# Performance work log

Hardware: AMD Instinct MI355X
Metric: run time of the kernel (lower is better)

The kernel has to match this reference:

```python
import jax, jax.numpy as jnp
import numpy as np
import math

B, LQ, S, D = 8, 4096, 77, 1024
H, HD = 16, 64
R, ALPHA = 192, 16.0
LORA_SCALE = ALPHA / R
N_SUBJ = 32


def setup_inputs() -> dict:
    key = jax.random.key(0)
    ks = jax.random.split(key, 16)
    w = 0.02
    return {
        "hidden_states": jax.random.normal(ks[0], (B, LQ, D), jnp.float32),
        "encoder_hidden_states": jax.random.normal(ks[1], (B, S, D), jnp.float32),
        "Wq": jax.random.normal(ks[2], (D, D), jnp.float32) * w,
        "Wk": jax.random.normal(ks[3], (D, D), jnp.float32) * w,
        "Wv": jax.random.normal(ks[4], (D, D), jnp.float32) * w,
        "Wo": jax.random.normal(ks[5], (D, D), jnp.float32) * w,
        "bo": jnp.zeros((D,), jnp.float32),
        "Ak": jax.random.normal(ks[6], (R, D), jnp.float32) * w,
        "Bk": jax.random.normal(ks[7], (D, R), jnp.float32) * w,
        "Av": jax.random.normal(ks[8], (R, D), jnp.float32) * w,
        "Bv": jax.random.normal(ks[9], (D, R), jnp.float32) * w,
        "Ao": jax.random.normal(ks[10], (R, D), jnp.float32) * w,
        "Bo": jax.random.normal(ks[11], (D, R), jnp.float32) * w,
        "cross_attn_scale_factor": jnp.ones((), jnp.float32),
        "subj_b": jax.random.randint(ks[12], (N_SUBJ,), 0, B, jnp.int32),
        "subj_n": jax.random.randint(ks[13], (N_SUBJ,), 0, S, jnp.int32),
    }


def _lora(x, A, Bm):
    # peft LoRA delta: scale * (x @ A^T) @ B^T
    return LORA_SCALE * ((x @ A.T) @ Bm.T)


def reference(hidden_states, encoder_hidden_states, Wq, Wk, Wv, Wo, bo,
              Ak, Bk, Av, Bv, Ao, Bo, cross_attn_scale_factor, subj_b, subj_n):
    hs, ehs = hidden_states, encoder_hidden_states
    # q_lora_updates_query=False -> query uses the base projection only
    q = hs @ Wq.T                                  # [B, LQ, D]
    k = ehs @ Wk.T + _lora(ehs, Ak, Bk)            # [B, S, D] (to_k_lora)
    v = ehs @ Wv.T + _lora(ehs, Av, Bv)            # [B, S, D] (to_v_lora)

    q = q.reshape(B, LQ, H, HD).transpose(0, 2, 1, 3)   # [B,H,LQ,HD]
    k = k.reshape(B, S, H, HD).transpose(0, 2, 1, 3)    # [B,H,S,HD]
    v = v.reshape(B, S, H, HD).transpose(0, 2, 1, 3)

    scale = 1.0 / math.sqrt(HD)
    attn_score = jnp.einsum('bhld,bhsd->bhls', q, k) * scale  # [B,H,LQ,S]

    # normalize_cross_attn: zero-center subject-token scores over query dim,
    # then rescale by the learned cross_attn_scale_factor.
    sub = attn_score[subj_b, :, :, subj_n]                    # [K,H,LQ]
    sub = (sub - sub.mean(axis=2, keepdims=True)) * cross_attn_scale_factor
    attn_score = attn_score.at[subj_b, :, :, subj_n].set(sub)

    attn_weight = jax.nn.softmax(attn_score, axis=-1)
    out = jnp.einsum('bhls,bhsd->bhld', attn_weight, v)       # [B,H,LQ,HD]
    out = out.transpose(0, 2, 1, 3).reshape(B, LQ, D)

    # to_out_lora: base out-proj (with bias) + LoRA delta; to_out[1] dropout = id
    out = out @ Wo.T + bo + _lora(out, Ao, Bo)
    return out
```

## Files before the change

### kernel.cpp

```cpp
#include <hip/hip_runtime.h>
#include <stdint.h>

#define B_     8
#define LQ_    4096
#define S_     77
#define SP_    80
#define D_     1024
#define H_     16
#define HD_    64
#define NC_    1280
#define NSUBJ_ 32

typedef __attribute__((ext_vector_type(4))) float  f4;
typedef __attribute__((ext_vector_type(8))) short  short8;
typedef __attribute__((ext_vector_type(8))) unsigned short us8;
typedef __attribute__((ext_vector_type(4))) unsigned short us4;

__device__ __forceinline__ unsigned short f2bf(float f) {
  union { float f; unsigned u; } x; x.f = f;
  unsigned r = x.u + 0x7FFFu + ((x.u >> 16) & 1u);
  return (unsigned short)(r >> 16);
}

__device__ __forceinline__ void gload16(const void* g, void* s) {
  __builtin_amdgcn_global_load_lds((const __attribute__((address_space(1))) void*)g,
                                   (__attribute__((address_space(3))) void*)s, 16, 0, 0);
}

__global__ __launch_bounds__(256) void k_hssum(const float* __restrict__ hs,
                                               float* __restrict__ part,
                                               unsigned short* __restrict__ hsb) {
  int b = blockIdx.y;
  size_t base = ((size_t)b * LQ_ + (size_t)blockIdx.x * 64) * D_ + threadIdx.x * 4;
  f4 acc = {0.f, 0.f, 0.f, 0.f};
  for (int l = 0; l < 64; ++l) {
    f4 v = *(const f4*)(hs + base + (size_t)l * D_);
    acc += v;
    if (hsb) {
      us4 o;
#pragma unroll
      for (int j = 0; j < 4; ++j) o[j] = f2bf(v[j]);
      *(us4*)(hsb + base + (size_t)l * D_) = o;
    }
  }
  *(f4*)(part + (size_t)blockIdx.x * (B_ * D_) + b * D_ + threadIdx.x * 4) = acc;
}

__global__ __launch_bounds__(256) void k_hsred(const float* __restrict__ part,
                                               float* __restrict__ hssum) {
  int i = blockIdx.x * 256 + threadIdx.x;
  float s = 0.f;
  for (int x = 0; x < 64; ++x) s += part[(size_t)x * (B_ * D_) + i];
  hssum[i] = s;
}

__global__ __launch_bounds__(256) void k_tr4(const float* __restrict__ Wq, const float* __restrict__ Ak,
                                             const float* __restrict__ Av, const float* __restrict__ Ao,
                                             float* __restrict__ wqT, float* __restrict__ akT,
                                             float* __restrict__ avT, float* __restrict__ aoT) {
  int z = blockIdx.z;
  const float* in = z == 0 ? Wq : (z == 1 ? Ak : (z == 2 ? Av : Ao));
  float* out = z == 0 ? wqT : (z == 1 ? akT : (z == 2 ? avT : aoT));
  int R = z == 0 ? 1024 : 192;
  const int C = 1024;
  int c0 = blockIdx.x * 32, r0 = blockIdx.y * 32;
  if (r0 >= R) return;
  __shared__ float tile[32][33];
  int tx = threadIdx.x & 31, ty = threadIdx.x >> 5;
#pragma unroll
  for (int k = 0; k < 4; ++k)
    tile[ty + 8 * k][tx] = in[(size_t)(r0 + ty + 8 * k) * C + c0 + tx];
  __syncthreads();
#pragma unroll
  for (int k = 0; k < 4; ++k)
    out[(size_t)(c0 + ty + 8 * k) * R + r0 + tx] = tile[tx][ty + 8 * k];
}

template <bool OBF>
__device__ __forceinline__ void gemm64_body(
    const float* __restrict__ A, int lda, const float* __restrict__ Bt, int ldb,
    void* __restrict__ Cv, int ldc, long cbase, const float* __restrict__ Dm, int ldd,
    int M, int Mv, int N, int K, float alpha, int m0, int n0,
    short* As, short* Bs) {
  int t = threadIdx.x, lane = t & 63, wid = t >> 6;
  int wm = wid >> 1, wn = wid & 1;
  f4 acc[2][2] = {};
  int srow = t >> 2, skc = (t & 3) * 8;
  for (int k0 = 0; k0 < K; k0 += 32) {
    __syncthreads();
    f4 a0 = {0,0,0,0}, a1 = {0,0,0,0}, b0 = {0,0,0,0}, b1 = {0,0,0,0};
    if (m0 + srow < Mv) {
      const float* p = A + (size_t)(m0 + srow) * lda + k0 + skc;
      a0 = *(const f4*)p; a1 = *(const f4*)(p + 4);
    }
    if (n0 + srow < N) {
      const float* p = Bt + (size_t)(n0 + srow) * ldb + k0 + skc;
      b0 = *(const f4*)p; b1 = *(const f4*)(p + 4);
    }
    us8 ua, ub;
#pragma unroll
    for (int j = 0; j < 4; ++j) {
      ua[j] = f2bf(a0[j]); ua[4 + j] = f2bf(a1[j]);
      ub[j] = f2bf(b0[j]); ub[4 + j] = f2bf(b1[j]);
    }
    *(us8*)(As + srow * 40 + skc) = ua;
    *(us8*)(Bs + srow * 40 + skc) = ub;
    __syncthreads();
    short8 fa[2], fb[2];
#pragma unroll
    for (int i = 0; i < 2; ++i) {
      fa[i] = *(const short8*)(As + (wm * 32 + i * 16 + (lane & 15)) * 40 + (lane >> 4) * 8);
      fb[i] = *(const short8*)(Bs + (wn * 32 + i * 16 + (lane & 15)) * 40 + (lane >> 4) * 8);
    }
#pragma unroll
    for (int mi = 0; mi < 2; ++mi)
#pragma unroll
      for (int ni = 0; ni < 2; ++ni)
        acc[mi][ni] = __builtin_amdgcn_mfma_f32_16x16x32_bf16(fa[mi], fb[ni], acc[mi][ni], 0, 0, 0);
  }
#pragma unroll
  for (int mi = 0; mi < 2; ++mi)
#pragma unroll
    for (int ni = 0; ni < 2; ++ni)
#pragma unroll
      for (int j = 0; j < 4; ++j) {
        int row = m0 + wm * 32 + mi * 16 + (lane >> 4) * 4 + j;
        int col = n0 + wn * 32 + ni * 16 + (lane & 15);
        if (row < M && col < N) {
          float val = acc[mi][ni][j] * alpha;
          if (Dm) val += Dm[(size_t)row * ldd + col];
          size_t idx = (size_t)cbase + (size_t)row * ldc + col;
          if (OBF) ((unsigned short*)Cv)[idx] = f2bf(val);
          else     ((float*)Cv)[idx] = val;
        }
      }
}

template <bool OBF>
__global__ __launch_bounds__(256) void k_gemm_small(
    const float* __restrict__ A, int lda, long sA1, long sA2,
    const float* __restrict__ Bt, int ldb, long sB1, long sB2,
    void* __restrict__ Cv, int ldc, long sC1, long sC2,
    const float* __restrict__ Dm, int ldd,
    int M, int Mv, int N, int K, float alpha, int Z2) {
  int z = blockIdx.z, z1 = z / Z2, z2 = z - z1 * Z2;
  __shared__ short As[64 * 40];
  __shared__ short Bs[64 * 40];
  gemm64_body<OBF>(A + z1 * sA1 + z2 * sA2, lda, Bt + z1 * sB1 + z2 * sB2, ldb,
                   Cv, ldc, z1 * sC1 + z2 * sC2, Dm, ldd, M, Mv, N, K, alpha,
                   blockIdx.x * 64, blockIdx.y * 64, As, Bs);
}

__global__ __launch_bounds__(256) void k_weff(
    const float* __restrict__ Bk, const float* __restrict__ Bv, const float* __restrict__ Bo,
    const float* __restrict__ akT, const float* __restrict__ avT, const float* __restrict__ aoT,
    const float* __restrict__ Wk, const float* __restrict__ Wv, const float* __restrict__ Wo,
    float* __restrict__ weff, float alpha) {
  int z = blockIdx.z;
  const float* A  = z == 0 ? Bk : (z == 1 ? Bv : Bo);
  const float* Bt = z == 0 ? akT : (z == 1 ? avT : aoT);
  const float* Dm = z == 0 ? Wk : (z == 1 ? Wv : Wo);
  __shared__ short As[64 * 40];
  __shared__ short Bs[64 * 40];
  gemm64_body<false>(A, 192, Bt, 192, weff + (size_t)z * 1048576, 1024, 0, Dm, 1024,
                     1024, 1024, 1024, 192, alpha, blockIdx.x * 64, blockIdx.y * 64, As, Bs);
}

__global__ void k_mubeta(const float* __restrict__ hssum, const float* __restrict__ Wq,
                         const float* __restrict__ kv,
                         const int* __restrict__ sb, const int* __restrict__ sn,
                         const float* __restrict__ csf_p,
                         float* __restrict__ alphav, float* __restrict__ betav) {
  int h = blockIdx.x, b = blockIdx.y;
  int t = threadIdx.x;
  __shared__ float qp[64];
  {
    int hd = t >> 1, half = t & 1;
    const float* wr = Wq + (size_t)(h * 64 + hd) * D_ + half * 512;
    const float* hp = hssum + b * D_ + half * 512;
    float s = 0.f;
    for (int d = 0; d < 512; d += 4) {
      f4 w = *(const f4*)(wr + d);
      f4 x = *(const f4*)(hp + d);
      s += w[0] * x[0] + w[1] * x[1] + w[2] * x[2] + w[3] * x[3];
    }
    s += __shfl_xor(s, 1, 64);
    if (half == 0) qp[hd] = s * (1.f / 4096.f);
  }
  __syncthreads();
  int s = t;
  if (s >= SP_) return;
  const float* kp = kv + ((size_t)(b * SP_ + s)) * 2048 + h * HD_;
  float mu = 0.f;
#pragma unroll 8
  for (int hd = 0; hd < HD_; ++hd) mu += qp[hd] * kp[hd];
  mu *= 0.125f;
  bool subj = false;
  for (int i = 0; i < NSUBJ_; ++i) subj = subj || (sb[i] == b && sn[i] == s);
  float csf = *csf_p;
  int c = b * NC_ + h * SP_ + s;
  alphav[c] = subj ? csf : 1.f;
  betav[c] = (s >= S_) ? -1e30f : (subj ? -mu * csf : 0.f);
}

__global__ __launch_bounds__(512, 4) void k_score_big(
    const unsigned short* __restrict__ hsb, const unsigned short* __restrict__ Mt,
    const float* __restrict__ alphav, const float* __restrict__ betav,
    unsigned short* __restrict__ P) {
  extern __shared__ short lds[];
  short* A0 = lds;
  short* B0 = lds + 16384;
  int id = blockIdx.x;
  int x = id & 7, idp = id >> 3;
  int nt = idp & 7;
  int pid = (idp >> 3) * 8 + x;
  int b = pid >> 4, mt = pid & 15;
  int m0 = mt * 256, n0 = nt * 160;

  const unsigned short* Ab = hsb + (size_t)b * LQ_ * D_;
  const unsigned short* Bb = Mt + (size_t)b * NC_ * D_;
  const float* alp = alphav + b * NC_;
  const float* bet = betav + b * NC_;
  unsigned short* Pb = P + (size_t)b * LQ_ * NC_;

  int t = threadIdx.x, lane = t & 63, wid = t >> 6;
  int wm = wid >> 1, wn = wid & 1;
  int r = lane & 15, q = lane >> 4;
  f4 acc[4][5] = {};

  auto SA = [&](int bf, int k0, int p) {
    int cb = p * 512 + wid * 64;
    int cc = cb + lane;
    int row = cc >> 2, gc = (cc & 3) ^ ((row >> 1) & 3);
    gload16(Ab + (size_t)(m0 + row) * D_ + k0 + gc * 8, (char*)(A0 + bf * 8192) + cb * 16);
  };
  auto SB = [&](int bf, int k0, int p) {
    int cb = p * 512 + wid * 64;
    int cc = cb + lane;
    int row = cc >> 2, gc = (cc & 3) ^ ((row >> 1) & 3);
    gload16(Bb + (size_t)(n0 + row) * D_ + k0 + gc * 8, (char*)(B0 + bf * 5120) + cb * 16);
  };
  auto STAGE = [&](int bf, int k0) {
    SA(bf, k0, 0); SA(bf, k0, 1);
    SB(bf, k0, 0);
    if (wid < 2) SB(bf, k0, 1);
  };

  STAGE(0, 0);
  int cur = 0;
  for (int kt = 0; kt < 32; ++kt) {
    if (kt < 31) {
      STAGE(cur ^ 1, (kt + 1) * 32);
      if (wid < 2) asm volatile("s_waitcnt vmcnt(4)" ::: "memory");
      else         asm volatile("s_waitcnt vmcnt(3)" ::: "memory");
    } else {
      asm volatile("s_waitcnt vmcnt(0)" ::: "memory");
    }
    __builtin_amdgcn_s_barrier();
    const short* Ar = A0 + cur * 8192;
    const short* Br = B0 + cur * 5120;
    short8 fa[4], fb[5];
#pragma unroll
    for (int ni = 0; ni < 5; ++ni) {
      int row = wn * 80 + ni * 16 + r;
      fb[ni] = *(const short8*)(Br + row * 32 + ((q ^ ((row >> 1) & 3)) * 8));
    }
#pragma unroll
    for (int mi = 0; mi < 4; ++mi) {
      int row = wm * 64 + mi * 16 + r;
      fa[mi] = *(const short8*)(Ar + row * 32 + ((q ^ ((row >> 1) & 3)) * 8));
    }
    __builtin_amdgcn_s_setprio(1);
#pragma unroll
    for (int mi = 0; mi < 4; ++mi)
#pragma unroll
      for (int ni = 0; ni < 5; ++ni)
        acc[mi][ni] = __builtin_amdgcn_mfma_f32_16x16x32_bf16(fa[mi], fb[ni], acc[mi][ni], 0, 0, 0);
    __builtin_amdgcn_s_setprio(0);
    __builtin_amdgcn_s_barrier();
    cur ^= 1;
  }

  float al[5], be[5];
#pragma unroll
  for (int ni = 0; ni < 5; ++ni) {
    int cc = n0 + wn * 80 + ni * 16 + r;
    al[ni] = alp[cc]; be[ni] = bet[cc];
  }
#pragma unroll
  for (int mi = 0; mi < 4; ++mi) {
#pragma unroll
    for (int j = 0; j < 4; ++j) {
      float v[5];
      float m = -3.0e38f;
#pragma unroll
      for (int ni = 0; ni < 5; ++ni) { v[ni] = acc[mi][ni][j] * al[ni] + be[ni]; m = fmaxf(m, v[ni]); }
#pragma unroll
      for (int off = 1; off < 16; off <<= 1) m = fmaxf(m, __shfl_xor(m, off, 64));
      float ssum = 0.f;
#pragma unroll
      for (int ni = 0; ni < 5; ++ni) { v[ni] = __expf(v[ni] - m); ssum += v[ni]; }
#pragma unroll
      for (int off = 1; off < 16; off <<= 1) ssum += __shfl_xor(ssum, off, 64);
      float inv = 1.f / ssum;
      int row = m0 + wm * 64 + mi * 16 + q * 4 + j;
      size_t rb = (size_t)row * NC_ + n0 + wn * 80 + r;
#pragma unroll
      for (int ni = 0; ni < 5; ++ni)
        Pb[rb + ni * 16] = f2bf(v[ni] * inv);
    }
  }
}

__global__ __launch_bounds__(256) void k_score_f32(
    const float* __restrict__ hs, const unsigned short* __restrict__ Mt,
    const float* __restrict__ alphav, const float* __restrict__ betav,
    unsigned short* __restrict__ P) {
  int id = blockIdx.x;
  int x = id & 7, idp = id >> 3;
  int n_t = idp & 7;
  int pid = (idp >> 3) * 8 + x;
  int b = pid >> 5, m_t = pid & 31;
  int m0 = m_t * 128, n0 = n_t * 160;
  const float* Af = hs + (size_t)b * LQ_ * D_;
  const unsigned short* Bb = Mt + (size_t)b * NC_ * D_;
  const float* alp = alphav + b * NC_;
  const float* bet = betav + b * NC_;
  unsigned short* Pb = P + (size_t)b * LQ_ * NC_;
  __shared__ short As[128 * 64];
  __shared__ short Bs[160 * 64];
  int t = threadIdx.x, lane = t & 63, wid = t >> 6;
  int wm = wid >> 1, wn = wid & 1;
  int srow = lane >> 3;
  int schunk = (lane & 7) ^ srow;
  f4 acc[4][5] = {};
  for (int k0 = 0; k0 < D_; k0 += 64) {
    __syncthreads();
    for (int i = wid; i < 20; i += 4)
      gload16(Bb + (size_t)(n0 + i * 8 + srow) * D_ + k0 + schunk * 8, (char*)Bs + i * 1024);
    int arow = t >> 3, ac = t & 7;
    int awc = ac ^ (arow & 7);
#pragma unroll
    for (int p = 0; p < 4; ++p) {
      int row = p * 32 + arow;
      const float* src = Af + (size_t)(m0 + row) * D_ + k0 + ac * 8;
      f4 v0 = *(const f4*)src;
      f4 v1 = *(const f4*)(src + 4);
      us8 u;
#pragma unroll
      for (int j = 0; j < 4; ++j) { u[j] = f2bf(v0[j]); u[4 + j] = f2bf(v1[j]); }
      *(us8*)(As + row * 64 + awc * 8) = u;
    }
    __syncthreads();
#pragma unroll
    for (int kk = 0; kk < 2; ++kk) {
      int co = ((kk * 4 + (lane >> 4)) ^ (lane & 7)) * 8;
      short8 fa[4], fb[5];
#pragma unroll
      for (int mi = 0; mi < 4; ++mi)
        fa[mi] = *(const short8*)(As + (wm * 64 + mi * 16 + (lane & 15)) * 64 + co);
#pragma unroll
      for (int ni = 0; ni < 5; ++ni)
        fb[ni] = *(const short8*)(Bs + (wn * 80 + ni * 16 + (lane & 15)) * 64 + co);
#pragma unroll
      for (int mi = 0; mi < 4; ++mi)
#pragma unroll
        for (int ni = 0; ni < 5; ++ni)
          acc[mi][ni] = __builtin_amdgcn_mfma_f32_16x16x32_bf16(fa[mi], fb[ni], acc[mi][ni], 0, 0, 0);
    }
  }
  float al[5], be[5];
#pragma unroll
  for (int ni = 0; ni < 5; ++ni) {
    int cc = n0 + wn * 80 + ni * 16 + (lane & 15);
    al[ni] = alp[cc]; be[ni] = bet[cc];
  }
#pragma unroll
  for (int mi = 0; mi < 4; ++mi) {
#pragma unroll
    for (int j = 0; j < 4; ++j) {
      float v[5];
      float m = -3.0e38f;
#pragma unroll
      for (int ni = 0; ni < 5; ++ni) { v[ni] = acc[mi][ni][j] * al[ni] + be[ni]; m = fmaxf(m, v[ni]); }
#pragma unroll
      for (int off = 1; off < 16; off <<= 1) m = fmaxf(m, __shfl_xor(m, off, 64));
      float ssum = 0.f;
#pragma unroll
      for (int ni = 0; ni < 5; ++ni) { v[ni] = __expf(v[ni] - m); ssum += v[ni]; }
#pragma unroll
      for (int off = 1; off < 16; off <<= 1) ssum += __shfl_xor(ssum, off, 64);
      float inv = 1.f / ssum;
      int row = m0 + wm * 64 + mi * 16 + (lane >> 4) * 4 + j;
      size_t rb = (size_t)row * NC_ + n0 + wn * 80 + (lane & 15);
#pragma unroll
      for (int ni = 0; ni < 5; ++ni)
        Pb[rb + ni * 16] = f2bf(v[ni] * inv);
    }
  }
}

__global__ __launch_bounds__(512, 4) void k_out_big(
    const unsigned short* __restrict__ P, const unsigned short* __restrict__ Ut,
    const float* __restrict__ bo, float* __restrict__ out) {
  extern __shared__ short lds[];
  short* A0 = lds;
  short* B0 = lds + 16384;
  int id = blockIdx.x;
  int x = id & 7, idp = id >> 3;
  int nt = idp & 7;
  int pid = (idp >> 3) * 8 + x;
  int b = pid >> 4, mt = pid & 15;
  int m0 = mt * 256, n0 = nt * 128;

  const unsigned short* Ab = P + (size_t)b * LQ_ * NC_;
  const unsigned short* Bb = Ut + (size_t)b * D_ * NC_;
  float* ob = out + (size_t)b * LQ_ * D_;

  int t = threadIdx.x, lane = t & 63, wid = t >> 6;
  int wm = wid >> 1, wn = wid & 1;
  int r = lane & 15, q = lane >> 4;
  f4 acc[4][4] = {};
  const int T = NC_ / 32;

  auto SA = [&](int bf, int k0, int p) {
    int cb = p * 512 + wid * 64;
    int cc = cb + lane;
    int row = cc >> 2, gc = (cc & 3) ^ ((row >> 1) & 3);
    gload16(Ab + (size_t)(m0 + row) * NC_ + k0 + gc * 8, (char*)(A0 + bf * 8192) + cb * 16);
  };
  auto SB = [&](int bf, int k0) {
    int cb = wid * 64;
    int cc = cb + lane;
    int row = cc >> 2, gc = (cc & 3) ^ ((row >> 1) & 3);
    gload16(Bb + (size_t)(n0 + row) * NC_ + k0 + gc * 8, (char*)(B0 + bf * 4096) + cb * 16);
  };
  auto STAGE = [&](int bf, int k0) { SA(bf, k0, 0); SA(bf, k0, 1); SB(bf, k0); };

  STAGE(0, 0);
  int cur = 0;
  for (int kt = 0; kt < T; ++kt) {
    if (kt + 1 < T) {
      STAGE(cur ^ 1, (kt + 1) * 32);
      asm volatile("s_waitcnt vmcnt(3)" ::: "memory");
    } else {
      asm volatile("s_waitcnt vmcnt(0)" ::: "memory");
    }
    __builtin_amdgcn_s_barrier();
    const short* Ar = A0 + cur * 8192;
    const short* Br = B0 + cur * 4096;
    short8 fa[4], fb[4];
#pragma unroll
    for (int ni = 0; ni < 4; ++ni) {
      int row = wn * 64 + ni * 16 + r;
      fb[ni] = *(const short8*)(Br + row * 32 + ((q ^ ((row >> 1) & 3)) * 8));
    }
#pragma unroll
    for (int mi = 0; mi < 4; ++mi) {
      int row = wm * 64 + mi * 16 + r;
      fa[mi] = *(const short8*)(Ar + row * 32 + ((q ^ ((row >> 1) & 3)) * 8));
    }
    __builtin_amdgcn_s_setprio(1);
#pragma unroll
    for (int mi = 0; mi < 4; ++mi)
#pragma unroll
      for (int ni = 0; ni < 4; ++ni)
        acc[mi][ni] = __builtin_amdgcn_mfma_f32_16x16x32_bf16(fa[mi], fb[ni], acc[mi][ni], 0, 0, 0);
    __builtin_amdgcn_s_setprio(0);
    __builtin_amdgcn_s_barrier();
    cur ^= 1;
  }

#pragma unroll
  for (int ni = 0; ni < 4; ++ni) {
    int col = n0 + wn * 64 + ni * 16 + r;
    float bov = bo[col];
#pragma unroll
    for (int mi = 0; mi < 4; ++mi)
#pragma unroll
      for (int j = 0; j < 4; ++j) {
        int row = m0 + wm * 64 + mi * 16 + q * 4 + j;
        ob[(size_t)row * D_ + col] = acc[mi][ni][j] + bov;
      }
  }
}

extern "C" void kernel_launch(void* const* d_in, const int* in_sizes, int n_in,
                              void* d_out, int out_size, void* d_ws, size_t ws_size,
                              hipStream_t stream) {
  const float* hs  = (const float*)d_in[0];
  const float* ehs = (const float*)d_in[1];
  const float* Wq  = (const float*)d_in[2];
  const float* Wk  = (const float*)d_in[3];
  const float* Wv  = (const float*)d_in[4];
  const float* Wo  = (const float*)d_in[5];
  const float* bo  = (const float*)d_in[6];
  const float* Ak  = (const float*)d_in[7];
  const float* Bk  = (const float*)d_in[8];
  const float* Av  = (const float*)d_in[9];
  const float* Bv  = (const float*)d_in[10];
  const float* Ao  = (const float*)d_in[11];
  const float* Bo  = (const float*)d_in[12];
  const float* csf = (const float*)d_in[13];
  const int*   sb  = (const int*)d_in[14];
  const int*   sn  = (const int*)d_in[15];
  float* out = (float*)d_out;

  hipFuncSetAttribute(reinterpret_cast<const void*>(k_score_big),
                      hipFuncAttributeMaxDynamicSharedMemorySize, 53248);
  hipFuncSetAttribute(reinterpret_cast<const void*>(k_out_big),
                      hipFuncAttributeMaxDynamicSharedMemorySize, 49152);

  char* ws = (char*)d_ws;
  unsigned short* P  = (unsigned short*)ws;
  unsigned short* Mt = (unsigned short*)(ws + 83886080);
  unsigned short* Ut = (unsigned short*)(ws + 104857600);
  const size_t NEED_HSB = 125829120ULL + 67108864ULL + 81920ULL;
  bool useHsb = ws_size >= NEED_HSB;
  unsigned short* hsb = useHsb ? (unsigned short*)(ws + 125829120) : nullptr;
  char* tail = useHsb ? (ws + 192937984) : (ws + 125829120);
  float* alphav = (float*)tail;
  float* betav  = (float*)(tail + 40960);
  float* kvbuf = (float*)(ws + 0);
  float* weff  = (float*)(ws + 5242880);
  float* wqT   = (float*)(ws + 17825792);
  float* aT    = (float*)(ws + 22020096);
  float* part  = (float*)(ws + 24379392);
  float* hssum = (float*)(ws + 26476544);

  float* woE = weff + 2097152;
  float* akT = aT;
  float* avT = aT + 196608;
  float* aoT = aT + 393216;

  const float LS = 16.0f / 192.0f;

  k_hssum<<<dim3(64, 8), 256, 0, stream>>>(hs, part, hsb);
  k_hsred<<<32, 256, 0, stream>>>(part, hssum);

  k_tr4<<<dim3(32, 32, 4), 256, 0, stream>>>(Wq, Ak, Av, Ao, wqT, akT, avT, aoT);

  k_weff<<<dim3(16, 16, 3), 256, 0, stream>>>(Bk, Bv, Bo, akT, avT, aoT, Wk, Wv, Wo, weff, LS);

  k_gemm_small<false><<<dim3(2, 32, 8), 256, 0, stream>>>(
      ehs, 1024, 77L * 1024, 0, weff, 1024, 0, 0, kvbuf, 2048, 80L * 2048, 0, nullptr, 0,
      80, 77, 2048, 1024, 1.f, 1);

  k_gemm_small<true><<<dim3(2, 16, 128), 256, 0, stream>>>(
      kvbuf, 2048, 80L * 2048, 64L, wqT, 1024, 0, 64L,
      Mt, 1024, (long)NC_ * 1024, 80L * 1024, nullptr, 0,
      80, 80, 1024, 64, 0.125f, 16);

  k_gemm_small<true><<<dim3(16, 2, 128), 256, 0, stream>>>(
      woE, 1024, 0, 64L, kvbuf + 1024, 2048, 80L * 2048, 64L,
      Ut, NC_, 1024L * NC_, 80L, nullptr, 0,
      1024, 1024, 80, 64, 1.f, 16);

  k_mubeta<<<dim3(16, 8), 128, 0, stream>>>(hssum, Wq, kvbuf, sb, sn, csf, alphav, betav);

  if (useHsb)
    k_score_big<<<1024, 512, 53248, stream>>>(hsb, Mt, alphav, betav, P);
  else
    k_score_f32<<<2048, 256, 0, stream>>>(hs, Mt, alphav, betav, P);
  k_out_big<<<1024, 512, 49152, stream>>>(P, Ut, bo, out);

  (void)in_sizes; (void)n_in; (void)out_size; (void)ws_size;
}
```

Before: 383.4 us.

## Enlarge score and output GEMM tiles and deepen the LDS pipeline to four stages

Both big bf16 GEMM kernels (score+softmax and output projection) switch to larger block tiles, 256x320 and 256x256, with 8 waves laid out 2x4. The per-wave M extent doubles, so each wave holds twice as many accumulators. The LDS double buffer becomes a 4-stage ring prefetching three k-steps ahead, with vmcnt waits adjusted per stage, and grid sizes are halved. The goal is more operand reuse per global load and better latency hiding. In exchange, LDS grows to 144KB and 128KB, which allows roughly one block per CU, and register pressure rises, so occupancy drops sharply and the 512-block grid gives only two waves over the CUs.

```diff
diff --git a/kernel.cpp b/kernel.cpp
--- a/kernel.cpp
+++ b/kernel.cpp
@@ -203,19 +203,17 @@
   betav[c] = (s >= S_) ? -1e30f : (subj ? -mu * csf : 0.f);
 }
 
-__global__ __launch_bounds__(512, 4) void k_score_big(
+__global__ __launch_bounds__(512, 2) void k_score_big(
     const unsigned short* __restrict__ hsb, const unsigned short* __restrict__ Mt,
     const float* __restrict__ alphav, const float* __restrict__ betav,
     unsigned short* __restrict__ P) {
   extern __shared__ short lds[];
-  short* A0 = lds;
-  short* B0 = lds + 16384;
   int id = blockIdx.x;
   int x = id & 7, idp = id >> 3;
-  int nt = idp & 7;
-  int pid = (idp >> 3) * 8 + x;
+  int nt = idp & 3;
+  int pid = (idp >> 2) * 8 + x;
   int b = pid >> 4, mt = pid & 15;
-  int m0 = mt * 256, n0 = nt * 160;
+  int m0 = mt * 256, n0 = nt * 320;
 
   const unsigned short* Ab = hsb + (size_t)b * LQ_ * D_;
   const unsigned short* Bb = Mt + (size_t)b * NC_ * D_;
@@ -224,61 +222,70 @@
   unsigned short* Pb = P + (size_t)b * LQ_ * NC_;
 
   int t = threadIdx.x, lane = t & 63, wid = t >> 6;
-  int wm = wid >> 1, wn = wid & 1;
+  int wm = wid >> 2, wn = wid & 3;
   int r = lane & 15, q = lane >> 4;
-  f4 acc[4][5] = {};
+  f4 acc[8][5] = {};
 
   auto SA = [&](int bf, int k0, int p) {
     int cb = p * 512 + wid * 64;
     int cc = cb + lane;
     int row = cc >> 2, gc = (cc & 3) ^ ((row >> 1) & 3);
-    gload16(Ab + (size_t)(m0 + row) * D_ + k0 + gc * 8, (char*)(A0 + bf * 8192) + cb * 16);
+    gload16(Ab + (size_t)(m0 + row) * D_ + k0 + gc * 8, (char*)(lds + bf * 8192) + cb * 16);
   };
   auto SB = [&](int bf, int k0, int p) {
     int cb = p * 512 + wid * 64;
     int cc = cb + lane;
     int row = cc >> 2, gc = (cc & 3) ^ ((row >> 1) & 3);
-    gload16(Bb + (size_t)(n0 + row) * D_ + k0 + gc * 8, (char*)(B0 + bf * 5120) + cb * 16);
+    gload16(Bb + (size_t)(n0 + row) * D_ + k0 + gc * 8, (char*)(lds + 32768 + bf * 10240) + cb * 16);
   };
   auto STAGE = [&](int bf, int k0) {
     SA(bf, k0, 0); SA(bf, k0, 1);
-    SB(bf, k0, 0);
-    if (wid < 2) SB(bf, k0, 1);
+    SB(bf, k0, 0); SB(bf, k0, 1);
+    if (wid < 4) { int cb = 1024 + wid * 64; int cc = cb + lane;
+      int row = cc >> 2, gc = (cc & 3) ^ ((row >> 1) & 3);
+      gload16(Bb + (size_t)(n0 + row) * D_ + k0 + gc * 8, (char*)(lds + 32768) + (size_t)bf * 20480 + cb * 16);
+    }
   };
 
-  STAGE(0, 0);
-  int cur = 0;
-  for (int kt = 0; kt < 32; ++kt) {
-    if (kt < 31) {
-      STAGE(cur ^ 1, (kt + 1) * 32);
-      if (wid < 2) asm volatile("s_waitcnt vmcnt(4)" ::: "memory");
-      else         asm volatile("s_waitcnt vmcnt(3)" ::: "memory");
+  const int T = 32;
+  STAGE(0, 0); STAGE(1, 32); STAGE(2, 64);
+  for (int kt = 0; kt < T; ++kt) {
+    if (kt + 3 < T) {
+      STAGE((kt + 3) & 3, (kt + 3) * 32);
+      if (wid < 4) asm volatile("s_waitcnt vmcnt(15)" ::: "memory");
+      else         asm volatile("s_waitcnt vmcnt(12)" ::: "memory");
+    } else if (kt + 2 < T) {
+      if (wid < 4) asm volatile("s_waitcnt vmcnt(10)" ::: "memory");
+      else         asm volatile("s_waitcnt vmcnt(8)" ::: "memory");
+    } else if (kt + 1 < T) {
+      if (wid < 4) asm volatile("s_waitcnt vmcnt(5)" ::: "memory");
+      else         asm volatile("s_waitcnt vmcnt(4)" ::: "memory");
     } else {
       asm volatile("s_waitcnt vmcnt(0)" ::: "memory");
     }
     __builtin_amdgcn_s_barrier();
-    const short* Ar = A0 + cur * 8192;
-    const short* Br = B0 + cur * 5120;
-    short8 fa[4], fb[5];
+    int cur = kt & 3;
+    const short* Ar = lds + cur * 8192;
+    const short* Br = lds + 32768 + cur * 10240;
+    short8 fa[8], fb[5];
 #pragma unroll
     for (int ni = 0; ni < 5; ++ni) {
       int row = wn * 80 + ni * 16 + r;
       fb[ni] = *(const short8*)(Br + row * 32 + ((q ^ ((row >> 1) & 3)) * 8));
     }
 #pragma unroll
-    for (int mi = 0; mi < 4; ++mi) {
-      int row = wm * 64 + mi * 16 + r;
+    for (int mi = 0; mi < 8; ++mi) {
+      int row = wm * 128 + mi * 16 + r;
       fa[mi] = *(const short8*)(Ar + row * 32 + ((q ^ ((row >> 1) & 3)) * 8));
     }
     __builtin_amdgcn_s_setprio(1);
 #pragma unroll
-    for (int mi = 0; mi < 4; ++mi)
+    for (int mi = 0; mi < 8; ++mi)
 #pragma unroll
       for (int ni = 0; ni < 5; ++ni)
         acc[mi][ni] = __builtin_amdgcn_mfma_f32_16x16x32_bf16(fa[mi], fb[ni], acc[mi][ni], 0, 0, 0);
     __builtin_amdgcn_s_setprio(0);
     __builtin_amdgcn_s_barrier();
-    cur ^= 1;
   }
 
   float al[5], be[5];
@@ -288,7 +295,7 @@
     al[ni] = alp[cc]; be[ni] = bet[cc];
   }
 #pragma unroll
-  for (int mi = 0; mi < 4; ++mi) {
+  for (int mi = 0; mi < 8; ++mi) {
 #pragma unroll
     for (int j = 0; j < 4; ++j) {
       float v[5];
@@ -303,7 +310,7 @@
 #pragma unroll
       for (int off = 1; off < 16; off <<= 1) ssum += __shfl_xor(ssum, off, 64);
       float inv = 1.f / ssum;
-      int row = m0 + wm * 64 + mi * 16 + q * 4 + j;
+      int row = m0 + wm * 128 + mi * 16 + q * 4 + j;
       size_t rb = (size_t)row * NC_ + n0 + wn * 80 + r;
 #pragma unroll
       for (int ni = 0; ni < 5; ++ni)
@@ -400,75 +407,76 @@
   }
 }
 
-__global__ __launch_bounds__(512, 4) void k_out_big(
+__global__ __launch_bounds__(512, 2) void k_out_big(
     const unsigned short* __restrict__ P, const unsigned short* __restrict__ Ut,
     const float* __restrict__ bo, float* __restrict__ out) {
   extern __shared__ short lds[];
-  short* A0 = lds;
-  short* B0 = lds + 16384;
   int id = blockIdx.x;
   int x = id & 7, idp = id >> 3;
-  int nt = idp & 7;
-  int pid = (idp >> 3) * 8 + x;
+  int nt = idp & 3;
+  int pid = (idp >> 2) * 8 + x;
   int b = pid >> 4, mt = pid & 15;
-  int m0 = mt * 256, n0 = nt * 128;
+  int m0 = mt * 256, n0 = nt * 256;
 
   const unsigned short* Ab = P + (size_t)b * LQ_ * NC_;
   const unsigned short* Bb = Ut + (size_t)b * D_ * NC_;
   float* ob = out + (size_t)b * LQ_ * D_;
 
   int t = threadIdx.x, lane = t & 63, wid = t >> 6;
-  int wm = wid >> 1, wn = wid & 1;
+  int wm = wid >> 2, wn = wid & 3;
   int r = lane & 15, q = lane >> 4;
-  f4 acc[4][4] = {};
+  f4 acc[8][4] = {};
   const int T = NC_ / 32;
 
   auto SA = [&](int bf, int k0, int p) {
     int cb = p * 512 + wid * 64;
     int cc = cb + lane;
     int row = cc >> 2, gc = (cc & 3) ^ ((row >> 1) & 3);
-    gload16(Ab + (size_t)(m0 + row) * NC_ + k0 + gc * 8, (char*)(A0 + bf * 8192) + cb * 16);
+    gload16(Ab + (size_t)(m0 + row) * NC_ + k0 + gc * 8, (char*)(lds + bf * 8192) + cb * 16);
   };
-  auto SB = [&](int bf, int k0) {
-    int cb = wid * 64;
+  auto SB = [&](int bf, int k0, int p) {
+    int cb = p * 512 + wid * 64;
     int cc = cb + lane;
     int row = cc >> 2, gc = (cc & 3) ^ ((row >> 1) & 3);
-    gload16(Bb + (size_t)(n0 + row) * NC_ + k0 + gc * 8, (char*)(B0 + bf * 4096) + cb * 16);
+    gload16(Bb + (size_t)(n0 + row) * NC_ + k0 + gc * 8, (char*)(lds + 32768 + bf * 8192) + cb * 16);
   };
-  auto STAGE = [&](int bf, int k0) { SA(bf, k0, 0); SA(bf, k0, 1); SB(bf, k0); };
-
-  STAGE(0, 0);
-  int cur = 0;
+  auto STAGE = [&](int bf, int k0) { SA(bf, k0, 0); SA(bf, k0, 1); SB(bf, k0, 0); SB(bf, k0, 1); };
+
+  STAGE(0, 0); STAGE(1, 32); STAGE(2, 64);
   for (int kt = 0; kt < T; ++kt) {
-    if (kt + 1 < T) {
-      STAGE(cur ^ 1, (kt + 1) * 32);
-      asm volatile("s_waitcnt vmcnt(3)" ::: "memory");
+    if (kt + 3 < T) {
+      STAGE((kt + 3) & 3, (kt + 3) * 32);
+      asm volatile("s_waitcnt vmcnt(12)" ::: "memory");
+    } else if (kt + 2 < T) {
+      asm volatile("s_waitcnt vmcnt(8)" ::: "memory");
+    } else if (kt + 1 < T) {
+      asm volatile("s_waitcnt vmcnt(4)" ::: "memory");
     } else {
       asm volatile("s_waitcnt vmcnt(0)" ::: "memory");
     }
     __builtin_amdgcn_s_barrier();
-    const short* Ar = A0 + cur * 8192;
-    const short* Br = B0 + cur * 4096;
-    short8 fa[4], fb[4];
+    int cur = kt & 3;
+    const short* Ar = lds + cur * 8192;
+    const short* Br = lds + 32768 + cur * 8192;
+    short8 fa[8], fb[4];
 #pragma unroll
     for (int ni = 0; ni < 4; ++ni) {
       int row = wn * 64 + ni * 16 + r;
       fb[ni] = *(const short8*)(Br + row * 32 + ((q ^ ((row >> 1) & 3)) * 8));
     }
 #pragma unroll
-    for (int mi = 0; mi < 4; ++mi) {
-      int row = wm * 64 + mi * 16 + r;
+    for (int mi = 0; mi < 8; ++mi) {
+      int row = wm * 128 + mi * 16 + r;
       fa[mi] = *(const short8*)(Ar + row * 32 + ((q ^ ((row >> 1) & 3)) * 8));
     }
     __builtin_amdgcn_s_setprio(1);
 #pragma unroll
-    for (int mi = 0; mi < 4; ++mi)
+    for (int mi = 0; mi < 8; ++mi)
 #pragma unroll
       for (int ni = 0; ni < 4; ++ni)
         acc[mi][ni] = __builtin_amdgcn_mfma_f32_16x16x32_bf16(fa[mi], fb[ni], acc[mi][ni], 0, 0, 0);
     __builtin_amdgcn_s_setprio(0);
     __builtin_amdgcn_s_barrier();
-    cur ^= 1;
   }
 
 #pragma unroll
@@ -476,10 +484,10 @@
     int col = n0 + wn * 64 + ni * 16 + r;
     float bov = bo[col];
 #pragma unroll
-    for (int mi = 0; mi < 4; ++mi)
+    for (int mi = 0; mi < 8; ++mi)
 #pragma unroll
       for (int j = 0; j < 4; ++j) {
-        int row = m0 + wm * 64 + mi * 16 + q * 4 + j;
+        int row = m0 + wm * 128 + mi * 16 + q * 4 + j;
         ob[(size_t)row * D_ + col] = acc[mi][ni][j] + bov;
       }
   }
@@ -507,9 +515,9 @@
   float* out = (float*)d_out;
 
   hipFuncSetAttribute(reinterpret_cast<const void*>(k_score_big),
-                      hipFuncAttributeMaxDynamicSharedMemorySize, 53248);
+                      hipFuncAttributeMaxDynamicSharedMemorySize, 147456);
   hipFuncSetAttribute(reinterpret_cast<const void*>(k_out_big),
-                      hipFuncAttributeMaxDynamicSharedMemorySize, 49152);
+                      hipFuncAttributeMaxDynamicSharedMemorySize, 131072);
 
   char* ws = (char*)d_ws;
   unsigned short* P  = (unsigned short*)ws;
@@ -559,10 +567,10 @@
   k_mubeta<<<dim3(16, 8), 128, 0, stream>>>(hssum, Wq, kvbuf, sb, sn, csf, alphav, betav);
 
   if (useHsb)
-    k_score_big<<<1024, 512, 53248, stream>>>(hsb, Mt, alphav, betav, P);
+    k_score_big<<<512, 512, 147456, stream>>>(hsb, Mt, alphav, betav, P);
   else
     k_score_f32<<<2048, 256, 0, stream>>>(hs, Mt, alphav, betav, P);
-  k_out_big<<<1024, 512, 49152, stream>>>(P, Ut, bo, out);
+  k_out_big<<<512, 512, 131072, stream>>>(P, Ut, bo, out);
 
   (void)in_sizes; (void)n_in; (void)out_size; (void)ws_size;
 }
```

After: 377.5 us (median of 2 runs). No clear change (-1.5%).
